# Performance work log

Measured on AMD Instinct MI355X. Metric: run time of the kernel, lower is better.

Reference implementation:

```python
import jax, jax.numpy as jnp
import numpy as np

B, H, N, D = 4, 16, 2048, 128  # batch, num_head, maxlen, head_dim (qkdim == vdim)
EPS = 1e-6


def _act(x):
    # '1+elu' kernel feature map
    return jax.nn.elu(x) + 1.0


def _simple_rms_norm(x):
    # SimpleRMSNorm over the last dim: x / sqrt(mean(x^2) + eps), no learned scale
    ms = jnp.mean(jnp.square(x), axis=-1, keepdims=True)
    return x * jax.lax.rsqrt(ms + EPS)


def setup_inputs() -> dict:
    key = jax.random.key(0)
    kq, kk, kv, km = jax.random.split(key, 4)
    Q = jax.random.normal(kq, (B, H, N, D), dtype=jnp.float32)
    K = jax.random.normal(kk, (B, H, N, D), dtype=jnp.float32)
    V = jax.random.normal(kv, (B, H, N, D), dtype=jnp.float32)
    mask = jax.random.uniform(km, (B, N), dtype=jnp.float32)
    return {"Q": Q, "K": K, "V": V, "mask": mask}


def reference(Q, K, V, mask):
    m = mask[:, None, :, None]           # (B, 1, N, 1)
    Qf = _act(Q)                          # (B, H, N, D)
    Kf = _act(K) * m                      # masked feature-mapped keys
    Vf = V * m                            # masked values
    # non-causal linear attention: KV = sum_n K_n (x) V_n ; out = Q @ KV
    KV = jnp.einsum('bhnd,bhne->bhde', Kf, Vf)    # (B, H, D, D)
    out = jnp.einsum('bhde,bhnd->bhne', KV, Qf)   # (B, H, N, D)
    return _simple_rms_norm(out)
```

## Files before the change

kernel.cpp:

```cpp
#include <hip/hip_runtime.h>
#include <hip/hip_bf16.h>

#define NBH 64
#define NSEQ 2048
#define DD 128
#define EPS 1e-6f

typedef __bf16 bf16x8 __attribute__((ext_vector_type(8)));
typedef __bf16 bf16x4 __attribute__((ext_vector_type(4)));
typedef float  f32x4  __attribute__((ext_vector_type(4)));

__device__ __forceinline__ float elu1(float x) {
    return x > 0.f ? x + 1.f : __expf(x);
}

__device__ __forceinline__ int swz(int r) {
    return ((r >> 2) & 7) ^ ((r & 1) << 2);
}

__global__ __launch_bounds__(512, 4) void kv_partial_kernel(
    const float* __restrict__ K, const float* __restrict__ V,
    const float* __restrict__ mask, float* __restrict__ part)
{
    __shared__ __bf16 KfT[128 * 128];
    __shared__ __bf16 VfT[128 * 128];

    const int s    = blockIdx.x;
    const int bh   = blockIdx.y;
    const int b    = bh >> 4;
    const int t    = threadIdx.x;
    const int c    = t & 31;
    const int rg   = t >> 5;
    const int lane = t & 63;
    const int w    = t >> 6;
    const int quad = lane >> 4;
    const int col  = lane & 15;
    const int n0   = s * 256;

    const f32x4* K4   = (const f32x4*)(K + ((size_t)bh * NSEQ + n0) * DD);
    const f32x4* V4   = (const f32x4*)(V + ((size_t)bh * NSEQ + n0) * DD);
    const float* mrow = mask + b * NSEQ + n0;

    f32x4 acc[8];
    #pragma unroll
    for (int nt = 0; nt < 8; ++nt) acc[nt] = (f32x4){0.f, 0.f, 0.f, 0.f};

    const int arow = w * 16 + col;
    const int aidx = (arow * 128) | (swz(arow) << 3);
    int bidx[8];
    #pragma unroll
    for (int nt = 0; nt < 8; ++nt) {
        int r = nt * 16 + col;
        bidx[nt] = (r * 128) | (swz(r) << 3);
    }

    f32x4 kr[8], vr[8];
    float mv[8];

    auto stage = [&]() {
        #pragma unroll
        for (int i = 0; i < 4; ++i) {
            bf16x8 kc, vc;
            #pragma unroll
            for (int j = 0; j < 8; ++j) {
                float m = mv[j];
                kc[j] = (__bf16)(elu1(kr[j][i]) * m);
                vc[j] = (__bf16)(vr[j][i] * m);
            }
            int d  = 4 * c + i;
            int wi = d * 128 + 8 * (rg ^ swz(d));
            *(bf16x8*)&KfT[wi] = kc;
            *(bf16x8*)&VfT[wi] = vc;
        }
    };

    auto mfma_tile = [&]() {
        #pragma unroll
        for (int kk = 0; kk < 4; ++kk) {
            int k0 = kk * 32 + quad * 8;
            bf16x8 a = *(bf16x8*)&VfT[aidx ^ k0];
            #pragma unroll
            for (int nt = 0; nt < 8; ++nt) {
                bf16x8 bb = *(bf16x8*)&KfT[bidx[nt] ^ k0];
                acc[nt] = __builtin_amdgcn_mfma_f32_16x16x32_bf16(a, bb, acc[nt], 0, 0, 0);
            }
        }
    };

    #pragma unroll
    for (int j = 0; j < 8; ++j) {
        int row = rg * 8 + j;
        kr[j] = K4[row * 32 + c];
        vr[j] = V4[row * 32 + c];
        mv[j] = mrow[row];
    }
    stage();
    __syncthreads();

    #pragma unroll
    for (int j = 0; j < 8; ++j) {
        int row = 128 + rg * 8 + j;
        kr[j] = K4[row * 32 + c];
        vr[j] = V4[row * 32 + c];
        mv[j] = mrow[row];
    }

    mfma_tile();
    __syncthreads();
    stage();
    __syncthreads();
    mfma_tile();

    float* po = part + (((size_t)bh * 8 + s) << 14);
    #pragma unroll
    for (int r = 0; r < 4; ++r) {
        int e = w * 16 + quad * 4 + r;
        #pragma unroll
        for (int nt = 0; nt < 8; ++nt)
            po[e * 128 + nt * 16 + col] = acc[nt][r];
    }
}

__global__ __launch_bounds__(256) void kv_reduce_kernel(
    const float* __restrict__ part, __bf16* __restrict__ kvt)
{
    int gid = blockIdx.x * 256 + threadIdx.x;
    int i   = gid * 4;
    int bh  = i >> 14;
    int ii  = i & 16383;
    const float* p = part + (((size_t)bh * 8) << 14) + ii;
    f32x4 sum = (f32x4){0.f, 0.f, 0.f, 0.f};
    #pragma unroll
    for (int s = 0; s < 8; ++s)
        sum += *(const f32x4*)(p + ((size_t)s << 14));
    bf16x4 o;
    o[0] = (__bf16)sum[0]; o[1] = (__bf16)sum[1];
    o[2] = (__bf16)sum[2]; o[3] = (__bf16)sum[3];
    *(bf16x4*)&kvt[i] = o;
}

__global__ __launch_bounds__(256, 4) void qkv_norm_kernel(
    const float* __restrict__ Q, const __bf16* __restrict__ kvt,
    float* __restrict__ out)
{
    __shared__ __bf16 KVT[128 * 136];

    const int bh   = blockIdx.y;
    const int row0 = blockIdx.x * 64;
    const int t    = threadIdx.x;
    const int lane = t & 63;
    const int w    = t >> 6;
    const int quad = lane >> 4;
    const int col  = lane & 15;

    const int row = row0 + w * 16 + col;
    const f32x4* q4 = (const f32x4*)(Q + ((size_t)bh * NSEQ + row) * DD);
    f32x4 qr[8];
    #pragma unroll
    for (int kk = 0; kk < 4; ++kk) {
        qr[2 * kk]     = q4[kk * 8 + quad * 2];
        qr[2 * kk + 1] = q4[kk * 8 + quad * 2 + 1];
    }

    {
        const __bf16* src = kvt + ((size_t)bh << 14);
        #pragma unroll
        for (int i = 0; i < 8; ++i) {
            int idx = i * 256 + t;
            int e   = idx >> 4;
            int dd  = (idx & 15) * 8;
            *(bf16x8*)&KVT[e * 136 + dd] = *(const bf16x8*)&src[e * 128 + dd];
        }
    }
    __syncthreads();

    bf16x8 a[4];
    #pragma unroll
    for (int kk = 0; kk < 4; ++kk) {
        #pragma unroll
        for (int h = 0; h < 2; ++h) {
            f32x4 q = qr[2 * kk + h];
            #pragma unroll
            for (int u = 0; u < 4; ++u)
                a[kk][h * 4 + u] = (__bf16)elu1(q[u]);
        }
    }

    f32x4 acc[8];
    #pragma unroll
    for (int et = 0; et < 8; ++et) acc[et] = (f32x4){0.f, 0.f, 0.f, 0.f};

    #pragma unroll
    for (int kk = 0; kk < 4; ++kk) {
        int k0 = kk * 32 + quad * 8;
        #pragma unroll
        for (int et = 0; et < 8; ++et) {
            bf16x8 bb = *(bf16x8*)&KVT[(et * 16 + col) * 136 + k0];
            acc[et] = __builtin_amdgcn_mfma_f32_16x16x32_bf16(a[kk], bb, acc[et], 0, 0, 0);
        }
    }

    float* ob = out + ((size_t)bh * NSEQ + row0) * DD;
    #pragma unroll
    for (int r = 0; r < 4; ++r) {
        float p = 0.f;
        #pragma unroll
        for (int et = 0; et < 8; ++et) p += acc[et][r] * acc[et][r];
        p += __shfl_xor(p, 1);
        p += __shfl_xor(p, 2);
        p += __shfl_xor(p, 4);
        p += __shfl_xor(p, 8);
        float scale = rsqrtf(p * (1.0f / 128.0f) + EPS);
        int orow = w * 16 + quad * 4 + r;
        #pragma unroll
        for (int et = 0; et < 8; ++et)
            ob[orow * DD + et * 16 + col] = acc[et][r] * scale;
    }
}

extern "C" void kernel_launch(void* const* d_in, const int* in_sizes, int n_in,
                              void* d_out, int out_size, void* d_ws, size_t ws_size,
                              hipStream_t stream) {
    const float* Q    = (const float*)d_in[0];
    const float* K    = (const float*)d_in[1];
    const float* V    = (const float*)d_in[2];
    const float* mask = (const float*)d_in[3];
    float* out = (float*)d_out;

    float*  part = (float*)d_ws;
    __bf16* kvt  = (__bf16*)((char*)d_ws + (size_t)NBH * 8 * 16384 * 4);

    kv_partial_kernel<<<dim3(8, NBH), 512, 0, stream>>>(K, V, mask, part);
    kv_reduce_kernel<<<1024, 256, 0, stream>>>(part, kvt);
    qkv_norm_kernel<<<dim3(32, NBH), 256, 0, stream>>>(Q, kvt, out);
}
```

Before: 251.1 us.

## Split K/V staging across half-blocks and double-buffer 64-row LDS tiles

The KV partial kernel now has the first 256 threads load and transform K while the other 256 handle V, instead of every thread doing both. The sequence chunk is processed as four 64-row tiles with double-buffered LDS, so the next tile's global loads overlap the current tile's MFMAs. Mask values are staged once through shared memory. The aim is to cut per-thread register pressure and hide global load latency, at the cost of more barriers and smaller MFMA bursts per synchronisation.

```diff
diff --git a/kernel.cpp b/kernel.cpp
--- a/kernel.cpp
+++ b/kernel.cpp
@@ -22,94 +22,100 @@
     const float* __restrict__ K, const float* __restrict__ V,
     const float* __restrict__ mask, float* __restrict__ part)
 {
-    __shared__ __bf16 KfT[128 * 128];
-    __shared__ __bf16 VfT[128 * 128];
+    __shared__ __bf16 KfT[2][128 * 64];
+    __shared__ __bf16 VfT[2][128 * 64];
+    __shared__ float  mloc[256];
 
     const int s    = blockIdx.x;
     const int bh   = blockIdx.y;
     const int b    = bh >> 4;
     const int t    = threadIdx.x;
-    const int c    = t & 31;
-    const int rg   = t >> 5;
     const int lane = t & 63;
     const int w    = t >> 6;
     const int quad = lane >> 4;
     const int col  = lane & 15;
     const int n0   = s * 256;
 
-    const f32x4* K4   = (const f32x4*)(K + ((size_t)bh * NSEQ + n0) * DD);
-    const f32x4* V4   = (const f32x4*)(V + ((size_t)bh * NSEQ + n0) * DD);
-    const float* mrow = mask + b * NSEQ + n0;
+    const int isV = t >> 8;
+    const int c   = t & 31;
+    const int rg  = (t >> 5) & 7;
+
+    const f32x4* S4 = (const f32x4*)((isV ? V : K) + ((size_t)bh * NSEQ + n0) * DD);
+    __bf16* myT = isV ? &VfT[0][0] : &KfT[0][0];
 
     f32x4 acc[8];
     #pragma unroll
     for (int nt = 0; nt < 8; ++nt) acc[nt] = (f32x4){0.f, 0.f, 0.f, 0.f};
 
     const int arow = w * 16 + col;
-    const int aidx = (arow * 128) | (swz(arow) << 3);
+    const int aidx = arow * 64 + (swz(arow) << 3);
     int bidx[8];
     #pragma unroll
     for (int nt = 0; nt < 8; ++nt) {
         int r = nt * 16 + col;
-        bidx[nt] = (r * 128) | (swz(r) << 3);
-    }
-
-    f32x4 kr[8], vr[8];
-    float mv[8];
-
-    auto stage = [&]() {
+        bidx[nt] = r * 64 + (swz(r) << 3);
+    }
+
+    f32x4 xr[8];
+
+    auto load_tile = [&](int tile) {
+        #pragma unroll
+        for (int j = 0; j < 8; ++j)
+            xr[j] = S4[(tile * 64 + rg * 8 + j) * 32 + c];
+    };
+
+    auto stage = [&](int buf, int tile) {
+        float ml[8];
+        #pragma unroll
+        for (int j = 0; j < 8; ++j) ml[j] = mloc[tile * 64 + rg * 8 + j];
+        __bf16* dst = myT + buf * (128 * 64);
         #pragma unroll
         for (int i = 0; i < 4; ++i) {
-            bf16x8 kc, vc;
-            #pragma unroll
-            for (int j = 0; j < 8; ++j) {
-                float m = mv[j];
-                kc[j] = (__bf16)(elu1(kr[j][i]) * m);
-                vc[j] = (__bf16)(vr[j][i] * m);
+            bf16x8 xc;
+            if (!isV) {
+                #pragma unroll
+                for (int j = 0; j < 8; ++j) xc[j] = (__bf16)(elu1(xr[j][i]) * ml[j]);
+            } else {
+                #pragma unroll
+                for (int j = 0; j < 8; ++j) xc[j] = (__bf16)(xr[j][i] * ml[j]);
             }
-            int d  = 4 * c + i;
-            int wi = d * 128 + 8 * (rg ^ swz(d));
-            *(bf16x8*)&KfT[wi] = kc;
-            *(bf16x8*)&VfT[wi] = vc;
+            int d = 4 * c + i;
+            *(bf16x8*)&dst[d * 64 + ((rg ^ swz(d)) << 3)] = xc;
         }
     };
 
-    auto mfma_tile = [&]() {
-        #pragma unroll
-        for (int kk = 0; kk < 4; ++kk) {
+    auto mfma_tile = [&](int buf) {
+        const __bf16* Vb = &VfT[buf][0];
+        const __bf16* Kb = &KfT[buf][0];
+        #pragma unroll
+        for (int kk = 0; kk < 2; ++kk) {
             int k0 = kk * 32 + quad * 8;
-            bf16x8 a = *(bf16x8*)&VfT[aidx ^ k0];
+            bf16x8 a = *(bf16x8*)&Vb[aidx ^ k0];
             #pragma unroll
             for (int nt = 0; nt < 8; ++nt) {
-                bf16x8 bb = *(bf16x8*)&KfT[bidx[nt] ^ k0];
+                bf16x8 bb = *(bf16x8*)&Kb[bidx[nt] ^ k0];
                 acc[nt] = __builtin_amdgcn_mfma_f32_16x16x32_bf16(a, bb, acc[nt], 0, 0, 0);
             }
         }
     };
 
-    #pragma unroll
-    for (int j = 0; j < 8; ++j) {
-        int row = rg * 8 + j;
-        kr[j] = K4[row * 32 + c];
-        vr[j] = V4[row * 32 + c];
-        mv[j] = mrow[row];
-    }
-    stage();
+    float mf = 0.f;
+    if (t < 256) mf = mask[b * NSEQ + n0 + t];
+    load_tile(0);
+    if (t < 256) mloc[t] = mf;
     __syncthreads();
-
-    #pragma unroll
-    for (int j = 0; j < 8; ++j) {
-        int row = 128 + rg * 8 + j;
-        kr[j] = K4[row * 32 + c];
-        vr[j] = V4[row * 32 + c];
-        mv[j] = mrow[row];
-    }
-
-    mfma_tile();
+    stage(0, 0);
     __syncthreads();
-    stage();
-    __syncthreads();
-    mfma_tile();
+
+    #pragma unroll
+    for (int tile = 0; tile < 4; ++tile) {
+        if (tile < 3) load_tile(tile + 1);
+        mfma_tile(tile & 1);
+        if (tile < 3) {
+            stage((tile + 1) & 1, tile + 1);
+            __syncthreads();
+        }
+    }
 
     float* po = part + (((size_t)bh * 8 + s) << 14);
     #pragma unroll
```

After: 236.6 us. 5.8% less time.
